# Performance work log

Hardware: AMD Instinct MI355X
Metric: run time of the kernel (lower is better)

Reference implementation:

```python
import jax, jax.numpy as jnp
import numpy as np

NUM_BINS = 256


def _equalize_channel(chan):
    # chan: (P,) int32 pixel values in [0, 255]. PIL/torchvision-style equalize.
    hist = jnp.zeros(NUM_BINS, jnp.float32).at[chan].add(1.0)
    total = hist.sum()
    # value of the last nonzero histogram bin (excluded from step computation)
    nz = hist > 0
    last_idx = (NUM_BINS - 1) - jnp.argmax(nz[::-1])
    last = hist[last_idx]
    step = jnp.floor((total - last) / 255.0)
    cum = jnpp_cumsum = jnp.cumsum(hist)
    lut = jnp.floor((cum + jnp.floor(step / 2.0)) / jnp.maximum(step, 1.0))
    # shift right by one (pad a leading 0, drop last) and clamp to [0,255]
    lut = jnp.clip(jnp.concatenate([jnp.zeros(1, jnp.float32), lut[:-1]]), 0.0, 255.0)
    ident = jnp.arange(NUM_BINS, dtype=jnp.float32)
    lut = jnp.where(step == 0, ident, lut)  # step==0 -> identity mapping
    return lut[chan]


def _equalize(x):
    # x: (N, C, H, W) float, pixel values -> uint8 semantics
    N, C, H, W = x.shape
    xi = jnp.clip(x, 0, 255).astype(jnp.int32).reshape(N * C, H * W)
    out = jax.vmap(_equalize_channel)(xi)  # (N*C, H*W) float32
    return out.reshape(N, C, H, W).astype(x.dtype)


def setup_inputs() -> dict:
    key = jax.random.key(0)
    x = jax.random.uniform(key, (64, 3, 512, 512), dtype=jnp.float32) * 255.0
    magnitude = 5
    return {"x": x, "magnitude": magnitude}


def reference(x, magnitude):
    # magnitude is unused in the original forward (Equalize ignores it)
    return _equalize(x)
```

## Files before the change

### kernel.cpp

```cpp
#include <hip/hip_runtime.h>

#define NBINS 256
#define HWPIX (512 * 512)
#define NCHAN (64 * 3)
#define HIST_BPC 8
#define APPLY_BPC 16
#define NCOPY 32

__global__ void zero_hist(int* __restrict__ hist) {
    hist[blockIdx.x * blockDim.x + threadIdx.x] = 0;
}

__global__ __launch_bounds__(256) void hist_kernel(const float* __restrict__ x,
                                                   int* __restrict__ hist) {
    __shared__ int lh[NBINS * NCOPY];
    const int chan = blockIdx.x / HIST_BPC;
    const int blk  = blockIdx.x % HIST_BPC;
    const int tid  = threadIdx.x;
    const int cp   = (tid & 63) >> 1;

    for (int i = tid; i < NBINS * NCOPY; i += 256) lh[i] = 0;
    __syncthreads();

    const float4* base = (const float4*)x + (size_t)chan * (HWPIX / 4);
    const int vecPerBlock = HWPIX / 4 / HIST_BPC;
    const int start = blk * vecPerBlock;

    for (int i = tid; i < vecPerBlock; i += 256) {
        float4 v = base[start + i];
        atomicAdd(&lh[(((int)fminf(fmaxf(v.x, 0.f), 255.f)) << 5) + cp], 1);
        atomicAdd(&lh[(((int)fminf(fmaxf(v.y, 0.f), 255.f)) << 5) + cp], 1);
        atomicAdd(&lh[(((int)fminf(fmaxf(v.z, 0.f), 255.f)) << 5) + cp], 1);
        atomicAdd(&lh[(((int)fminf(fmaxf(v.w, 0.f), 255.f)) << 5) + cp], 1);
    }
    __syncthreads();

    int s = 0;
    #pragma unroll
    for (int k = 0; k < NCOPY; ++k) {
        int c = (tid + k) & (NCOPY - 1);
        s += lh[(tid << 5) + c];
    }
    if (s) atomicAdd(&hist[chan * NBINS + tid], s);
}

__global__ __launch_bounds__(256) void apply_kernel(const float* __restrict__ x,
                                                    float* __restrict__ out,
                                                    const int* __restrict__ hist) {
    __shared__ int scan[NBINS];
    __shared__ float slut[NBINS * NCOPY];
    __shared__ int s_last_idx;
    __shared__ int s_last;

    const int chan = blockIdx.x / APPLY_BPC;
    const int blk  = blockIdx.x % APPLY_BPC;
    const int tid  = threadIdx.x;
    const int cp   = (tid & 63) >> 1;

    const int h = hist[chan * NBINS + tid];
    scan[tid] = h;
    if (tid == 0) s_last_idx = 0;
    __syncthreads();
    if (h > 0) atomicMax(&s_last_idx, tid);

    for (int off = 1; off < NBINS; off <<= 1) {
        __syncthreads();
        int t = (tid >= off) ? scan[tid - off] : 0;
        __syncthreads();
        scan[tid] += t;
    }
    __syncthreads();
    if (tid == s_last_idx) s_last = h;
    __syncthreads();

    const int total = scan[NBINS - 1];
    const int step  = (total - s_last) / 255;

    float lutv;
    if (step == 0) {
        lutv = (float)tid;
    } else if (tid == 0) {
        lutv = 0.f;
    } else {
        int l = (scan[tid - 1] + (step >> 1)) / step;
        lutv = (float)(l < 255 ? l : 255);
    }
    #pragma unroll
    for (int k = 0; k < NCOPY; ++k) {
        int c = (tid + k) & (NCOPY - 1);
        slut[(tid << 5) + c] = lutv;
    }
    __syncthreads();

    const float4* bx = (const float4*)x + (size_t)chan * (HWPIX / 4);
    float4*       bo = (float4*)out + (size_t)chan * (HWPIX / 4);
    const int vecPerBlock = HWPIX / 4 / APPLY_BPC;
    const int start = blk * vecPerBlock;

    for (int i = tid; i < vecPerBlock; i += 256) {
        float4 v = bx[start + i];
        float4 o;
        o.x = slut[(((int)fminf(fmaxf(v.x, 0.f), 255.f)) << 5) + cp];
        o.y = slut[(((int)fminf(fmaxf(v.y, 0.f), 255.f)) << 5) + cp];
        o.z = slut[(((int)fminf(fmaxf(v.z, 0.f), 255.f)) << 5) + cp];
        o.w = slut[(((int)fminf(fmaxf(v.w, 0.f), 255.f)) << 5) + cp];
        bo[start + i] = o;
    }
}

extern "C" void kernel_launch(void* const* d_in, const int* in_sizes, int n_in,
                              void* d_out, int out_size, void* d_ws, size_t ws_size,
                              hipStream_t stream) {
    const float* x = (const float*)d_in[0];
    float* out = (float*)d_out;
    int* hist = (int*)d_ws;

    zero_hist<<<NCHAN, NBINS, 0, stream>>>(hist);
    hist_kernel<<<NCHAN * HIST_BPC, 256, 0, stream>>>(x, hist);
    apply_kernel<<<NCHAN * APPLY_BPC, 256, 0, stream>>>(x, out, hist);
}
```

Before: 379.0 us.

## Pack clamped pixel bytes in histogram pass and apply LUT from packed buffer

```diff
diff --git a/kernel.cpp b/kernel.cpp
--- a/kernel.cpp
+++ b/kernel.cpp
@@ -1,63 +1,66 @@
 #include <hip/hip_runtime.h>
 
 #define NBINS 256
-#define HWPIX (512 * 512)
-#define NCHAN (64 * 3)
+#define NCHAN 192
 #define HIST_BPC 8
 #define APPLY_BPC 16
+#define TPB 256
+#define VEC_PER_CHAN (512 * 512 / 4)
 #define NCOPY 32
 
-__global__ void zero_hist(int* __restrict__ hist) {
-    hist[blockIdx.x * blockDim.x + threadIdx.x] = 0;
-}
-
-__global__ __launch_bounds__(256) void hist_kernel(const float* __restrict__ x,
-                                                   int* __restrict__ hist) {
+__global__ __launch_bounds__(TPB) void hist_pack(const float* __restrict__ x,
+                                                 unsigned* __restrict__ packed,
+                                                 int* __restrict__ partials) {
     __shared__ int lh[NBINS * NCOPY];
     const int chan = blockIdx.x / HIST_BPC;
     const int blk  = blockIdx.x % HIST_BPC;
     const int tid  = threadIdx.x;
     const int cp   = (tid & 63) >> 1;
 
-    for (int i = tid; i < NBINS * NCOPY; i += 256) lh[i] = 0;
+    for (int i = tid; i < NBINS * NCOPY; i += TPB) lh[i] = 0;
     __syncthreads();
 
-    const float4* base = (const float4*)x + (size_t)chan * (HWPIX / 4);
-    const int vecPerBlock = HWPIX / 4 / HIST_BPC;
-    const int start = blk * vecPerBlock;
+    const int vecPerBlock = VEC_PER_CHAN / HIST_BPC;
+    const size_t base = (size_t)chan * VEC_PER_CHAN + blk * vecPerBlock;
+    const float4* bx = (const float4*)x + base;
+    unsigned* bp = packed + base;
 
-    for (int i = tid; i < vecPerBlock; i += 256) {
-        float4 v = base[start + i];
-        atomicAdd(&lh[(((int)fminf(fmaxf(v.x, 0.f), 255.f)) << 5) + cp], 1);
-        atomicAdd(&lh[(((int)fminf(fmaxf(v.y, 0.f), 255.f)) << 5) + cp], 1);
-        atomicAdd(&lh[(((int)fminf(fmaxf(v.z, 0.f), 255.f)) << 5) + cp], 1);
-        atomicAdd(&lh[(((int)fminf(fmaxf(v.w, 0.f), 255.f)) << 5) + cp], 1);
+    for (int i = tid; i < vecPerBlock; i += TPB) {
+        float4 v = bx[i];
+        int a = (int)fminf(fmaxf(v.x, 0.f), 255.f);
+        int b = (int)fminf(fmaxf(v.y, 0.f), 255.f);
+        int c = (int)fminf(fmaxf(v.z, 0.f), 255.f);
+        int d = (int)fminf(fmaxf(v.w, 0.f), 255.f);
+        bp[i] = (unsigned)(a | (b << 8) | (c << 16) | (d << 24));
+        atomicAdd(&lh[(a << 5) + cp], 1);
+        atomicAdd(&lh[(b << 5) + cp], 1);
+        atomicAdd(&lh[(c << 5) + cp], 1);
+        atomicAdd(&lh[(d << 5) + cp], 1);
     }
     __syncthreads();
 
     int s = 0;
     #pragma unroll
-    for (int k = 0; k < NCOPY; ++k) {
-        int c = (tid + k) & (NCOPY - 1);
-        s += lh[(tid << 5) + c];
-    }
-    if (s) atomicAdd(&hist[chan * NBINS + tid], s);
+    for (int k = 0; k < NCOPY; ++k) s += lh[(tid << 5) + ((tid + k) & 31)];
+    partials[(chan * HIST_BPC + blk) * NBINS + tid] = s;
 }
 
-__global__ __launch_bounds__(256) void apply_kernel(const float* __restrict__ x,
+__global__ __launch_bounds__(TPB) void apply_kernel(const unsigned* __restrict__ packed,
                                                     float* __restrict__ out,
-                                                    const int* __restrict__ hist) {
+                                                    const int* __restrict__ partials) {
     __shared__ int scan[NBINS];
     __shared__ float slut[NBINS * NCOPY];
-    __shared__ int s_last_idx;
-    __shared__ int s_last;
+    __shared__ int s_last_idx, s_last;
 
     const int chan = blockIdx.x / APPLY_BPC;
     const int blk  = blockIdx.x % APPLY_BPC;
     const int tid  = threadIdx.x;
     const int cp   = (tid & 63) >> 1;
 
-    const int h = hist[chan * NBINS + tid];
+    int h = 0;
+    #pragma unroll
+    for (int b = 0; b < HIST_BPC; ++b)
+        h += partials[(chan * HIST_BPC + b) * NBINS + tid];
     scan[tid] = h;
     if (tid == 0) s_last_idx = 0;
     __syncthreads();
@@ -77,34 +80,29 @@
     const int step  = (total - s_last) / 255;
 
     float lutv;
-    if (step == 0) {
-        lutv = (float)tid;
-    } else if (tid == 0) {
-        lutv = 0.f;
-    } else {
+    if (step == 0)      lutv = (float)tid;
+    else if (tid == 0)  lutv = 0.f;
+    else {
         int l = (scan[tid - 1] + (step >> 1)) / step;
         lutv = (float)(l < 255 ? l : 255);
     }
     #pragma unroll
-    for (int k = 0; k < NCOPY; ++k) {
-        int c = (tid + k) & (NCOPY - 1);
-        slut[(tid << 5) + c] = lutv;
-    }
+    for (int k = 0; k < NCOPY; ++k) slut[(tid << 5) + ((tid + k) & 31)] = lutv;
     __syncthreads();
 
-    const float4* bx = (const float4*)x + (size_t)chan * (HWPIX / 4);
-    float4*       bo = (float4*)out + (size_t)chan * (HWPIX / 4);
-    const int vecPerBlock = HWPIX / 4 / APPLY_BPC;
-    const int start = blk * vecPerBlock;
+    const int vecPerBlock = VEC_PER_CHAN / APPLY_BPC;
+    const size_t base = (size_t)chan * VEC_PER_CHAN + blk * vecPerBlock;
+    const unsigned* bp = packed + base;
+    float4* bo = (float4*)out + base;
 
-    for (int i = tid; i < vecPerBlock; i += 256) {
-        float4 v = bx[start + i];
+    for (int i = tid; i < vecPerBlock; i += TPB) {
+        unsigned p = bp[i];
         float4 o;
-        o.x = slut[(((int)fminf(fmaxf(v.x, 0.f), 255.f)) << 5) + cp];
-        o.y = slut[(((int)fminf(fmaxf(v.y, 0.f), 255.f)) << 5) + cp];
-        o.z = slut[(((int)fminf(fmaxf(v.z, 0.f), 255.f)) << 5) + cp];
-        o.w = slut[(((int)fminf(fmaxf(v.w, 0.f), 255.f)) << 5) + cp];
-        bo[start + i] = o;
+        o.x = slut[(int)((p & 255u) << 5) + cp];
+        o.y = slut[(int)(((p >> 8) & 255u) << 5) + cp];
+        o.z = slut[(int)(((p >> 16) & 255u) << 5) + cp];
+        o.w = slut[(int)((p >> 24) << 5) + cp];
+        bo[i] = o;
     }
 }
 
@@ -113,9 +111,10 @@
                               hipStream_t stream) {
     const float* x = (const float*)d_in[0];
     float* out = (float*)d_out;
-    int* hist = (int*)d_ws;
 
-    zero_hist<<<NCHAN, NBINS, 0, stream>>>(hist);
-    hist_kernel<<<NCHAN * HIST_BPC, 256, 0, stream>>>(x, hist);
-    apply_kernel<<<NCHAN * APPLY_BPC, 256, 0, stream>>>(x, out, hist);
+    unsigned* packed = (unsigned*)d_ws;
+    int* partials = (int*)d_ws + (size_t)NCHAN * VEC_PER_CHAN;
+
+    hist_pack<<<NCHAN * HIST_BPC, TPB, 0, stream>>>(x, packed, partials);
+    apply_kernel<<<NCHAN * APPLY_BPC, TPB, 0, stream>>>(packed, out, partials);
 }
```

New measurement: 376.6 us. Within noise of the previous version (-0.6%).
